# Performance work log

Hardware: AMD Instinct MI355X
Metric: run time of the kernel (lower is better)

Reference implementation:

```python
import jax, jax.numpy as jnp
import numpy as np

NUM_LAYERS = 3
BUFFER_SIZE = 5
RECENCY = 0.9
LOW_POWER_K = 8

B, N, S, C = 8, 8192, 64, 16


def setup_inputs() -> dict:
    key = jax.random.key(0)
    ks = jax.random.split(key, 8)
    return {
        "x": jax.random.normal(ks[0], (B, N, S), jnp.float32),
        "entanglement": jax.random.normal(ks[1], (N, S), jnp.float32),
        # mixing initialized as identity in the module; perturb slightly so it is non-trivial
        "mixing": jnp.eye(N, dtype=jnp.float32) + 0.01 * jax.random.normal(ks[2], (N, N), jnp.float32),
        "readout_w": jax.random.normal(ks[3], (S, S), jnp.float32) / np.sqrt(S).astype(np.float32),
        "enc_w": jax.random.normal(ks[4], (C, S), jnp.float32) / np.sqrt(S).astype(np.float32),
        "enc_b": jnp.zeros((C,), jnp.float32),
        "dec_w": jax.random.normal(ks[5], (S, C), jnp.float32) / np.sqrt(C).astype(np.float32),
        "dec_b": jnp.zeros((S,), jnp.float32),
    }


def _temporal_proximity_scaling(stack, recency_factor):
    # stack: [T, N, S] of buffered activations, stack[-1] most recent.
    # Recency-weighted mean: most recent weight 1, older decayed by recency_factor.
    T = stack.shape[0]
    w = recency_factor ** jnp.arange(T - 1, -1, -1, dtype=stack.dtype)  # [T]
    return jnp.einsum('t,tns->ns', w, stack) / jnp.sum(w)


def _low_power_collapse(s, k):
    # keep top-k |values| per neuron row, zero the rest
    a = jnp.abs(s)
    vals, _ = jax.lax.top_k(a, k)           # [N, k]
    thr = vals[:, -1:]                       # kth largest magnitude per row
    return jnp.where(a >= thr, s, jnp.zeros_like(s))


def reference(x, entanglement, mixing, readout_w, enc_w, enc_b, dec_w, dec_b):
    gate = jax.nn.sigmoid(entanglement)[None]  # [1, N, S]
    buf = []  # ShortTermBuffer contents, vectorized over all neurons: list of [N, S]
    ns = jnp.zeros((N, S), x.dtype)
    for _ in range(NUM_LAYERS):
        # NOTE: the torch code prunes/decays/resets neuron_states at the top of each
        # layer but immediately overwrites it with x.mean(0) -> dead code, omitted.
        x = x * gate
        x = jnp.einsum('bns,nm->bms', x, mixing)
        ns = jnp.mean(x, axis=0)  # [N, S]
        buf.append(ns)
        buf = buf[-BUFFER_SIZE:]
        stack = jnp.stack(buf, axis=0)        # [T, N, S], T = min(layer+1, BUFFER_SIZE)
        ns = _temporal_proximity_scaling(stack, RECENCY)
        # advanced_state_collapse via autoencoder (importance_threshold=0.0 -> always reconstruct)
        h = jax.nn.relu(ns @ enc_w.T + enc_b)  # [N, C]
        ns = h @ dec_w.T + dec_b               # [N, S]
        ns = _low_power_collapse(ns, LOW_POWER_K)
    out = x @ readout_w.T  # Linear(S, S, bias=False)
    # torch forward returns only readout(x); neuron_states is a mutated buffer.
    # We also return it so the memory-bound per-neuron state pipeline is not DCE'd.
    return out, ns
```

## Files before the change

kernel.cpp:

```cpp
#include <hip/hip_runtime.h>

#define NN 8192
#define SS 64
#define BSD 512
#define NS (NN*SS)
#define NBS (NN*BSD)

typedef __attribute__((ext_vector_type(4))) _Float16 f16x4;
typedef __attribute__((ext_vector_type(8))) _Float16 f16x8;
typedef __attribute__((ext_vector_type(4))) float f32x4;

#define GLOAD_LDS16(gptr, lptr) \
    __builtin_amdgcn_global_load_lds((const __attribute__((address_space(1))) void*)(gptr), \
                                     (__attribute__((address_space(3))) void*)(lptr), 16, 0, 0)

__device__ __forceinline__ int kmap(int lane, int e) {
    return ((lane >> 4) << 2) + (e & 3) + ((e >> 2) << 4);
}

__global__ void sigmoid_gate_kernel(const float* __restrict__ ent, float* __restrict__ gate) {
    int i = blockIdx.x * 256 + threadIdx.x;
    gate[i] = 1.0f / (1.0f + expf(-ent[i]));
}

__global__ __launch_bounds__(256) void convA_kernel(const float* __restrict__ Mx,
                                                    char* __restrict__ Ab) {
    __shared__ _Float16 Lh[64][136];
    __shared__ _Float16 Ll[64][136];
    const int t = threadIdx.x;
    const int kt = blockIdx.x, mt = blockIdx.y;
    const int k0 = kt * 64, m0 = mt * 128;
    #pragma unroll
    for (int i = 0; i < 8; ++i) {
        int e = i * 256 + t;
        int kr = e >> 5, m4 = (e & 31) << 2;
        float4 v = *(const float4*)&Mx[(size_t)(k0 + kr) * NN + m0 + m4];
        int d = (k0 + kr) - (m0 + m4);
        if (d == 0) v.x -= 1.0f;
        if (d == 1) v.y -= 1.0f;
        if (d == 2) v.z -= 1.0f;
        if (d == 3) v.w -= 1.0f;
        f16x4 h, l;
        h[0] = (_Float16)v.x; l[0] = (_Float16)(v.x - (float)h[0]);
        h[1] = (_Float16)v.y; l[1] = (_Float16)(v.y - (float)h[1]);
        h[2] = (_Float16)v.z; l[2] = (_Float16)(v.z - (float)h[2]);
        h[3] = (_Float16)v.w; l[3] = (_Float16)(v.w - (float)h[3]);
        *(f16x4*)&Lh[kr][m4] = h;
        *(f16x4*)&Ll[kr][m4] = l;
    }
    __syncthreads();
    #pragma unroll
    for (int j = 0; j < 4; ++j) {
        int idx  = j * 256 + t;
        int h    = idx >> 9;
        int w    = idx & 511;
        int blk  = w >> 7;
        int kk   = (w >> 6) & 1;
        int lane = w & 63;
        int col  = h * 64 + blk * 16 + (lane & 15);
        int kb   = kk * 32;
        f16x8 hv, lv;
        #pragma unroll
        for (int e = 0; e < 8; ++e) {
            int k = kb + kmap(lane, e);
            hv[e] = Lh[k][col];
            lv[e] = Ll[k][col];
        }
        char* tile = Ab + (((size_t)(mt * 2 + h) * 128 + kt) << 14);
        *(f16x8*)(tile + w * 16)        = hv;
        *(f16x8*)(tile + 8192 + w * 16) = lv;
    }
}

__device__ __forceinline__ void pack_B(const _Float16 (*Lh)[520],
                                       const _Float16 (*Nh)[72], const _Float16 (*Nl)[72],
                                       char* Bb, char* Nb, int kt, int t) {
    #pragma unroll
    for (int j = 0; j < 16; ++j) {
        int idx = j * 256 + t;
        int nbt = idx >> 10, w = idx & 1023;
        int blk = w >> 7, kk = (w >> 6) & 1, lane = w & 63;
        int col = nbt * 128 + blk * 16 + (lane & 15);
        int kb = kk * 32;
        f16x8 hv;
        #pragma unroll
        for (int e = 0; e < 8; ++e)
            hv[e] = Lh[kb + kmap(lane, e)][col];
        *(f16x8*)(Bb + (((size_t)kt * 4 + nbt) << 14) + w * 16) = hv;
    }
    #pragma unroll
    for (int j = 0; j < 4; ++j) {
        int idx = j * 256 + t;
        int nbt = idx >> 8, r = idx & 255;
        int part = r >> 7, kk = (r >> 6) & 1, lane = r & 63;
        int s = nbt * 16 + (lane & 15);
        int kb = kk * 32;
        f16x8 v;
        #pragma unroll
        for (int e = 0; e < 8; ++e) {
            int k = kb + kmap(lane, e);
            v[e] = part ? Nl[k][s] : Nh[k][s];
        }
        *(f16x8*)(Nb + (((size_t)kt * 4 + nbt) << 12) + part * 2048 + kk * 1024 + lane * 16) = v;
    }
}

__global__ __launch_bounds__(256) void prep0_kernel(const float* __restrict__ x,
                                                    const float* __restrict__ gate,
                                                    float* __restrict__ X,
                                                    char* __restrict__ Bb,
                                                    char* __restrict__ Nb,
                                                    float* __restrict__ mg32) {
    __shared__ _Float16 Lh[64][520];
    __shared__ _Float16 Nh[64][72];
    __shared__ _Float16 Nl[64][72];
    const int t = threadIdx.x;
    const int kt = blockIdx.x;
    const int n0 = kt * 64;
    #pragma unroll
    for (int i = 0; i < 4; ++i) {
        int e = i * 256 + t;
        int kr = e >> 4;
        int s4 = (e & 15) << 2;
        float4 g = *(const float4*)&gate[(size_t)(n0 + kr) * 64 + s4];
        float4 ms = make_float4(0.f, 0.f, 0.f, 0.f);
        #pragma unroll
        for (int b = 0; b < 8; ++b) {
            float4 v = *(const float4*)&x[((size_t)b * NN + n0 + kr) * 64 + s4];
            ms.x += v.x; ms.y += v.y; ms.z += v.z; ms.w += v.w;
            v.x *= g.x; v.y *= g.y; v.z *= g.z; v.w *= g.w;
            *(float4*)&X[(size_t)(n0 + kr) * BSD + b * 64 + s4] = v;
            f16x4 h;
            h[0] = (_Float16)v.x; h[1] = (_Float16)v.y;
            h[2] = (_Float16)v.z; h[3] = (_Float16)v.w;
            *(f16x4*)&Lh[kr][b * 64 + s4] = h;
        }
        float4 mg4;
        mg4.x = ms.x * 0.125f * g.x; mg4.y = ms.y * 0.125f * g.y;
        mg4.z = ms.z * 0.125f * g.z; mg4.w = ms.w * 0.125f * g.w;
        *(float4*)&mg32[(size_t)(n0 + kr) * 64 + s4] = mg4;
        f16x4 mh, ml;
        mh[0] = (_Float16)mg4.x; ml[0] = (_Float16)(mg4.x - (float)mh[0]);
        mh[1] = (_Float16)mg4.y; ml[1] = (_Float16)(mg4.y - (float)mh[1]);
        mh[2] = (_Float16)mg4.z; ml[2] = (_Float16)(mg4.z - (float)mh[2]);
        mh[3] = (_Float16)mg4.w; ml[3] = (_Float16)(mg4.w - (float)mh[3]);
        *(f16x4*)&Nh[kr][s4] = mh;
        *(f16x4*)&Nl[kr][s4] = ml;
    }
    __syncthreads();
    pack_B(Lh, Nh, Nl, Bb, Nb, kt, t);
}

__global__ __launch_bounds__(256) void gateconv_kernel(float* __restrict__ X,
                                                       const float* __restrict__ gate,
                                                       const float* __restrict__ nsprev,
                                                       char* __restrict__ Bb,
                                                       char* __restrict__ Nb,
                                                       float* __restrict__ mg32) {
    __shared__ _Float16 Lh[64][520];
    __shared__ _Float16 Nh[64][72];
    __shared__ _Float16 Nl[64][72];
    const int t = threadIdx.x;
    const int kt = blockIdx.x;
    const int n0 = kt * 64;
    #pragma unroll
    for (int i = 0; i < 32; ++i) {
        int e = i * 256 + t;
        int kr = e >> 7;
        int c4 = (e & 127) << 2;
        float4 v = *(const float4*)&X[(size_t)(n0 + kr) * BSD + c4];
        float4 g = *(const float4*)&gate[(size_t)(n0 + kr) * 64 + (c4 & 63)];
        v.x *= g.x; v.y *= g.y; v.z *= g.z; v.w *= g.w;
        *(float4*)&X[(size_t)(n0 + kr) * BSD + c4] = v;
        f16x4 h;
        h[0] = (_Float16)v.x; h[1] = (_Float16)v.y;
        h[2] = (_Float16)v.z; h[3] = (_Float16)v.w;
        *(f16x4*)&Lh[kr][c4] = h;
    }
    #pragma unroll
    for (int i = 0; i < 4; ++i) {
        int e = i * 256 + t;
        int kr = e >> 4;
        int s4 = (e & 15) << 2;
        float4 p = *(const float4*)&nsprev[(size_t)(n0 + kr) * 64 + s4];
        float4 g = *(const float4*)&gate[(size_t)(n0 + kr) * 64 + s4];
        float4 mg4;
        mg4.x = p.x * g.x; mg4.y = p.y * g.y; mg4.z = p.z * g.z; mg4.w = p.w * g.w;
        *(float4*)&mg32[(size_t)(n0 + kr) * 64 + s4] = mg4;
        f16x4 mh, ml;
        mh[0] = (_Float16)mg4.x; ml[0] = (_Float16)(mg4.x - (float)mh[0]);
        mh[1] = (_Float16)mg4.y; ml[1] = (_Float16)(mg4.y - (float)mh[1]);
        mh[2] = (_Float16)mg4.z; ml[2] = (_Float16)(mg4.z - (float)mh[2]);
        mh[3] = (_Float16)mg4.w; ml[3] = (_Float16)(mg4.w - (float)mh[3]);
        *(f16x4*)&Nh[kr][s4] = mh;
        *(f16x4*)&Nl[kr][s4] = ml;
    }
    __syncthreads();
    pack_B(Lh, Nh, Nl, Bb, Nb, kt, t);
}

__global__ __launch_bounds__(256) void gemm_f16_kernel(const char* __restrict__ Ab,
                                                       const char* __restrict__ Bb,
                                                       const char* __restrict__ Nb,
                                                       float* X,
                                                       const float* __restrict__ mg,
                                                       float* __restrict__ nsout) {
    __shared__ char lds[2][20480];
    const int t = threadIdx.x;
    const int L = blockIdx.x;
    const int mt  = (L & 7) + ((L >> 5) << 3);
    const int nbt = (L >> 3) & 3;
    const int lane = t & 63, wid = t >> 6;

    const char* gA = Ab + (((size_t)mt * 128) << 14) + wid * 2048 + lane * 16;
    const char* gB = Bb + (((size_t)nbt) << 14) + wid * 4096 + lane * 16;
    const char* gN = Nb + (((size_t)nbt) << 12) + wid * 1024 + lane * 16;
    const uint32_t lA = wid * 2048;
    const uint32_t lN = 16384 + wid * 1024;

    auto stageA = [&](char* la, const char* pA, const char* pN) {
        GLOAD_LDS16(pA,               la + lA);
        GLOAD_LDS16(pA + 1024,        la + lA + 1024);
        GLOAD_LDS16(pA + 8192,        la + lA + 8192);
        GLOAD_LDS16(pA + 8192 + 1024, la + lA + 8192 + 1024);
        GLOAD_LDS16(pN,               la + lN);
    };

    f16x8 B0[4], B1[4];
    auto loadB = [&](f16x8* Br, const char* pB) {
        Br[0] = *(const f16x8*)(pB);
        Br[1] = *(const f16x8*)(pB + 1024);
        Br[2] = *(const f16x8*)(pB + 2048);
        Br[3] = *(const f16x8*)(pB + 3072);
    };

    f32x4 accm[4][2];
    #pragma unroll
    for (int fi = 0; fi < 4; ++fi) {
        accm[fi][0] = (f32x4){0.f, 0.f, 0.f, 0.f};
        accm[fi][1] = (f32x4){0.f, 0.f, 0.f, 0.f};
    }
    f32x4 accn = (f32x4){0.f, 0.f, 0.f, 0.f};

    auto compute = [&](const char* base, const f16x8* Br) {
        const char* A_ = base + lane * 16;
        const char* Bn = base + 16384 + lane * 16;
        #pragma unroll
        for (int kk = 0; kk < 2; ++kk) {
            const int ko = kk * 1024;
            f16x8 bnh = *(const f16x8*)(Bn + ko);
            f16x8 bnl = *(const f16x8*)(Bn + 2048 + ko);
            #pragma unroll
            for (int fi = 0; fi < 4; ++fi) {
                f16x8 ah = *(const f16x8*)(A_ + fi * 2048 + ko);
                accm[fi][0] = __builtin_amdgcn_mfma_f32_16x16x32_f16(ah, Br[kk],     accm[fi][0], 0, 0, 0);
                accm[fi][1] = __builtin_amdgcn_mfma_f32_16x16x32_f16(ah, Br[2 + kk], accm[fi][1], 0, 0, 0);
                if (fi == wid) {
                    f16x8 aln = *(const f16x8*)(A_ + 8192 + fi * 2048 + ko);
                    accn = __builtin_amdgcn_mfma_f32_16x16x32_f16(ah,  bnh, accn, 0, 0, 0);
                    accn = __builtin_amdgcn_mfma_f32_16x16x32_f16(ah,  bnl, accn, 0, 0, 0);
                    accn = __builtin_amdgcn_mfma_f32_16x16x32_f16(aln, bnh, accn, 0, 0, 0);
                }
            }
        }
    };

    stageA(lds[0], gA, gN);
    loadB(B0, gB);
    gA += 16384; gN += 16384; gB += 65536;

    for (int u = 0; u < 64; ++u) {
        asm volatile("s_waitcnt vmcnt(0)" ::: "memory");
        __builtin_amdgcn_s_barrier();
        __builtin_amdgcn_sched_barrier(0);
        stageA(lds[1], gA, gN);
        loadB(B1, gB);
        gA += 16384; gN += 16384; gB += 65536;
        __builtin_amdgcn_sched_barrier(0);
        compute(lds[0], B0);
        asm volatile("s_waitcnt vmcnt(0)" ::: "memory");
        __builtin_amdgcn_s_barrier();
        __builtin_amdgcn_sched_barrier(0);
        if (u < 63) {
            stageA(lds[0], gA, gN);
            loadB(B0, gB);
            gA += 16384; gN += 16384; gB += 65536;
        }
        __builtin_amdgcn_sched_barrier(0);
        compute(lds[1], B1);
    }

    const int row0 = mt * 64 + ((lane >> 4) << 2);
    const int col0 = nbt * 128 + wid * 32 + (lane & 15);
    #pragma unroll
    for (int fi = 0; fi < 4; ++fi)
        #pragma unroll
        for (int fj = 0; fj < 2; ++fj)
            #pragma unroll
            for (int j = 0; j < 4; ++j) {
                size_t idx = (size_t)(row0 + fi * 16 + j) * BSD + col0 + fj * 16;
                X[idx] = accm[fi][fj][j] + X[idx];
            }
    const int nr0 = mt * 64 + wid * 16 + ((lane >> 4) << 2);
    const int nc  = nbt * 16 + (lane & 15);
    #pragma unroll
    for (int j = 0; j < 4; ++j) {
        size_t nidx = (size_t)(nr0 + j) * 64 + nc;
        nsout[nidx] = accn[j] + mg[nidx];
    }
}

__global__ __launch_bounds__(256) void readout_kernel(const float* __restrict__ X3,
                                                      const float* __restrict__ W,
                                                      float* __restrict__ out) {
    __shared__ float Wt[64][65];
    __shared__ float xr[512];
    const int n = blockIdx.x;
    const int t = threadIdx.x;
    for (int e = t; e < 4096; e += 256) {
        int s = e >> 6, sp = e & 63;
        Wt[sp][s] = W[e];
    }
    xr[t]       = X3[(size_t)n * BSD + t];
    xr[t + 256] = X3[(size_t)n * BSD + 256 + t];
    __syncthreads();
    const int b1 = t >> 6;
    const int s  = t & 63;
    float acc0 = 0.0f, acc1 = 0.0f;
    #pragma unroll
    for (int sp = 0; sp < 64; ++sp) {
        float w = Wt[sp][s];
        acc0 += w * xr[b1 * 64 + sp];
        acc1 += w * xr[(b1 + 4) * 64 + sp];
    }
    out[((size_t)b1 * NN + n) * SS + s]       = acc0;
    out[((size_t)(b1 + 4) * NN + n) * SS + s] = acc1;
}

__global__ void nsfinal_kernel(const float* __restrict__ ns0,
                               const float* __restrict__ enc_w, const float* __restrict__ enc_b,
                               const float* __restrict__ dec_w, const float* __restrict__ dec_b,
                               float* __restrict__ out_ns) {
    int gtid = blockIdx.x * 256 + threadIdx.x;
    int lane = gtid & 63;
    const float r = 0.9f;
    const float wsum = 1.0f + r + r * r;
    float tns = (ns0[gtid] * (r * r) + ns0[NS + gtid] * r + ns0[2 * NS + gtid]) / wsum;
    float v = dec_b[lane];
    #pragma unroll
    for (int c = 0; c < 16; ++c) {
        float p = tns * enc_w[c * 64 + lane];
        #pragma unroll
        for (int off = 32; off; off >>= 1) p += __shfl_xor(p, off, 64);
        float h = fmaxf(p + enc_b[c], 0.0f);
        v += h * dec_w[lane * 16 + c];
    }
    float av = fabsf(v);
    int cnt = 0;
    for (int j = 0; j < 64; ++j) {
        float o = __shfl(av, j, 64);
        cnt += (o > av) ? 1 : 0;
    }
    out_ns[gtid] = (cnt < 8) ? v : 0.0f;
}

extern "C" void kernel_launch(void* const* d_in, const int* in_sizes, int n_in,
                              void* d_out, int out_size, void* d_ws, size_t ws_size,
                              hipStream_t stream) {
    const float* x      = (const float*)d_in[0];
    const float* ent    = (const float*)d_in[1];
    const float* mixing = (const float*)d_in[2];
    const float* r_w    = (const float*)d_in[3];
    const float* enc_w  = (const float*)d_in[4];
    const float* enc_b  = (const float*)d_in[5];
    const float* dec_w  = (const float*)d_in[6];
    const float* dec_b  = (const float*)d_in[7];
    float* out = (float*)d_out;

    char*  Ab   = (char*)d_ws;
    char*  Bb   = Ab + 268435456ull;
    char*  Nb   = Bb + 8388608ull;
    float* X    = (float*)(Nb + 2097152ull);
    float* mg32 = X + NBS;
    float* ns0  = mg32 + NS;
    float* gate = ns0 + 3 * (size_t)NS;

    sigmoid_gate_kernel<<<NS / 256, 256, 0, stream>>>(ent, gate);
    convA_kernel<<<dim3(128, 64), 256, 0, stream>>>(mixing, Ab);
    prep0_kernel<<<128, 256, 0, stream>>>(x, gate, X, Bb, Nb, mg32);

    for (int l = 0; l < 3; ++l) {
        gemm_f16_kernel<<<512, 256, 0, stream>>>(Ab, Bb, Nb, X, mg32, ns0 + (size_t)l * NS);
        if (l < 2)
            gateconv_kernel<<<128, 256, 0, stream>>>(X, gate, ns0 + (size_t)l * NS, Bb, Nb, mg32);
    }

    readout_kernel<<<NN, 256, 0, stream>>>(X, r_w, out);
    nsfinal_kernel<<<2048, 256, 0, stream>>>(ns0, enc_w, enc_b, dec_w, dec_b, out + NBS);
}
```

Measured before the change: 702.9 us.

## Split-K the mixing GEMM into two partial halves reduced downstream

Each layer's mixing GEMM is split along K into two halves, launched as 1024 blocks instead of 512 to raise occupancy. Each half writes fp32 partials, which the following gateconv, readout and nsfinal kernels sum together with the residual. The ns path is restructured to keep the full and low-precision halves in registers rather than LDS. This adds extra partial-buffer traffic and needs more workspace, with the old in-place path kept as a fallback when the workspace is too small.

```diff
diff --git a/kernel.cpp b/kernel.cpp
--- a/kernel.cpp
+++ b/kernel.cpp
@@ -152,11 +152,15 @@
 }
 
 __global__ __launch_bounds__(256) void gateconv_kernel(float* __restrict__ X,
+                                                       const float* __restrict__ P0,
+                                                       const float* __restrict__ P1,
                                                        const float* __restrict__ gate,
-                                                       const float* __restrict__ nsprev,
+                                                       float* __restrict__ mg32,
+                                                       const float* __restrict__ Np0,
+                                                       const float* __restrict__ Np1,
+                                                       float* __restrict__ nsf,
                                                        char* __restrict__ Bb,
-                                                       char* __restrict__ Nb,
-                                                       float* __restrict__ mg32) {
+                                                       char* __restrict__ Nb) {
     __shared__ _Float16 Lh[64][520];
     __shared__ _Float16 Nh[64][72];
     __shared__ _Float16 Nl[64][72];
@@ -168,10 +172,19 @@
         int e = i * 256 + t;
         int kr = e >> 7;
         int c4 = (e & 127) << 2;
-        float4 v = *(const float4*)&X[(size_t)(n0 + kr) * BSD + c4];
+        size_t idx = (size_t)(n0 + kr) * BSD + c4;
+        float4 v = *(const float4*)&X[idx];
+        if (P0) {
+            float4 p = *(const float4*)&P0[idx];
+            v.x += p.x; v.y += p.y; v.z += p.z; v.w += p.w;
+        }
+        if (P1) {
+            float4 p = *(const float4*)&P1[idx];
+            v.x += p.x; v.y += p.y; v.z += p.z; v.w += p.w;
+        }
         float4 g = *(const float4*)&gate[(size_t)(n0 + kr) * 64 + (c4 & 63)];
         v.x *= g.x; v.y *= g.y; v.z *= g.z; v.w *= g.w;
-        *(float4*)&X[(size_t)(n0 + kr) * BSD + c4] = v;
+        *(float4*)&X[idx] = v;
         f16x4 h;
         h[0] = (_Float16)v.x; h[1] = (_Float16)v.y;
         h[2] = (_Float16)v.z; h[3] = (_Float16)v.w;
@@ -182,11 +195,24 @@
         int e = i * 256 + t;
         int kr = e >> 4;
         int s4 = (e & 15) << 2;
-        float4 p = *(const float4*)&nsprev[(size_t)(n0 + kr) * 64 + s4];
-        float4 g = *(const float4*)&gate[(size_t)(n0 + kr) * 64 + s4];
+        size_t nidx = (size_t)(n0 + kr) * 64 + s4;
+        float4 p;
+        if (Np0) {
+            p = *(const float4*)&mg32[nidx];
+            float4 a = *(const float4*)&Np0[nidx];
+            p.x += a.x; p.y += a.y; p.z += a.z; p.w += a.w;
+            if (Np1) {
+                float4 b2 = *(const float4*)&Np1[nidx];
+                p.x += b2.x; p.y += b2.y; p.z += b2.z; p.w += b2.w;
+            }
+            *(float4*)&nsf[nidx] = p;
+        } else {
+            p = *(const float4*)&nsf[nidx];
+        }
+        float4 g = *(const float4*)&gate[nidx];
         float4 mg4;
         mg4.x = p.x * g.x; mg4.y = p.y * g.y; mg4.z = p.z * g.z; mg4.w = p.w * g.w;
-        *(float4*)&mg32[(size_t)(n0 + kr) * 64 + s4] = mg4;
+        *(float4*)&mg32[nidx] = mg4;
         f16x4 mh, ml;
         mh[0] = (_Float16)mg4.x; ml[0] = (_Float16)(mg4.x - (float)mh[0]);
         mh[1] = (_Float16)mg4.y; ml[1] = (_Float16)(mg4.y - (float)mh[1]);
@@ -199,25 +225,139 @@
     pack_B(Lh, Nh, Nl, Bb, Nb, kt, t);
 }
 
-__global__ __launch_bounds__(256) void gemm_f16_kernel(const char* __restrict__ Ab,
-                                                       const char* __restrict__ Bb,
-                                                       const char* __restrict__ Nb,
-                                                       float* X,
-                                                       const float* __restrict__ mg,
-                                                       float* __restrict__ nsout) {
+__global__ __launch_bounds__(256, 4) void gemm_split_kernel(const char* __restrict__ Ab,
+                                                            const char* __restrict__ Bb,
+                                                            const char* __restrict__ Nb,
+                                                            float* __restrict__ Pp,
+                                                            float* __restrict__ Npp) {
+    __shared__ char lds[2][16384];
+    const int t = threadIdx.x;
+    int L = blockIdx.x;
+    const int kb = L >> 9;
+    L &= 511;
+    const int mt  = (L & 7) + ((L >> 5) << 3);
+    const int nbt = (L >> 3) & 3;
+    const int lane = t & 63, wid = t >> 6;
+    const int kt0 = kb * 64;
+
+    const char* gA = Ab + (((size_t)mt * 128 + kt0) << 14) + wid * 2048 + lane * 16;
+    const char* gB = Bb + (((size_t)kt0 * 4 + nbt) << 14) + wid * 4096 + lane * 16;
+    const char* gN = Nb + (((size_t)kt0 * 4 + nbt) << 12) + lane * 16;
+    const uint32_t lA = wid * 2048;
+
+    auto stageA = [&](char* la, const char* pA) {
+        GLOAD_LDS16(pA,               la + lA);
+        GLOAD_LDS16(pA + 1024,        la + lA + 1024);
+        GLOAD_LDS16(pA + 8192,        la + lA + 8192);
+        GLOAD_LDS16(pA + 8192 + 1024, la + lA + 8192 + 1024);
+    };
+
+    f16x8 B0[4], B1[4];
+    auto loadB = [&](f16x8* Br, const char* pB) {
+        Br[0] = *(const f16x8*)(pB);
+        Br[1] = *(const f16x8*)(pB + 1024);
+        Br[2] = *(const f16x8*)(pB + 2048);
+        Br[3] = *(const f16x8*)(pB + 3072);
+    };
+    f16x8 N0[4], N1[4];
+    auto loadN = [&](f16x8* Nr, const char* pN) {
+        Nr[0] = *(const f16x8*)(pN);
+        Nr[1] = *(const f16x8*)(pN + 1024);
+        Nr[2] = *(const f16x8*)(pN + 2048);
+        Nr[3] = *(const f16x8*)(pN + 3072);
+    };
+
+    f32x4 accm[4][2];
+    #pragma unroll
+    for (int fi = 0; fi < 4; ++fi) {
+        accm[fi][0] = (f32x4){0.f, 0.f, 0.f, 0.f};
+        accm[fi][1] = (f32x4){0.f, 0.f, 0.f, 0.f};
+    }
+    f32x4 accn = (f32x4){0.f, 0.f, 0.f, 0.f};
+
+    auto compute = [&](const char* base, const f16x8* Br, const f16x8* Nr) {
+        const char* A_ = base + lane * 16;
+        #pragma unroll
+        for (int kk = 0; kk < 2; ++kk) {
+            const int ko = kk * 1024;
+            #pragma unroll
+            for (int fi = 0; fi < 4; ++fi) {
+                f16x8 ah = *(const f16x8*)(A_ + fi * 2048 + ko);
+                accm[fi][0] = __builtin_amdgcn_mfma_f32_16x16x32_f16(ah, Br[kk],     accm[fi][0], 0, 0, 0);
+                accm[fi][1] = __builtin_amdgcn_mfma_f32_16x16x32_f16(ah, Br[2 + kk], accm[fi][1], 0, 0, 0);
+                if (fi == wid) {
+                    f16x8 aln = *(const f16x8*)(A_ + 8192 + fi * 2048 + ko);
+                    accn = __builtin_amdgcn_mfma_f32_16x16x32_f16(ah,  Nr[kk],     accn, 0, 0, 0);
+                    accn = __builtin_amdgcn_mfma_f32_16x16x32_f16(ah,  Nr[2 + kk], accn, 0, 0, 0);
+                    accn = __builtin_amdgcn_mfma_f32_16x16x32_f16(aln, Nr[kk],     accn, 0, 0, 0);
+                }
+            }
+        }
+    };
+
+    stageA(lds[0], gA);
+    loadB(B0, gB);
+    loadN(N0, gN);
+    gA += 16384; gB += 65536; gN += 16384;
+
+    for (int u = 0; u < 32; ++u) {
+        asm volatile("s_waitcnt vmcnt(0)" ::: "memory");
+        __builtin_amdgcn_s_barrier();
+        __builtin_amdgcn_sched_barrier(0);
+        stageA(lds[1], gA);
+        loadB(B1, gB);
+        loadN(N1, gN);
+        gA += 16384; gB += 65536; gN += 16384;
+        __builtin_amdgcn_sched_barrier(0);
+        compute(lds[0], B0, N0);
+        asm volatile("s_waitcnt vmcnt(0)" ::: "memory");
+        __builtin_amdgcn_s_barrier();
+        __builtin_amdgcn_sched_barrier(0);
+        if (u < 31) {
+            stageA(lds[0], gA);
+            loadB(B0, gB);
+            loadN(N0, gN);
+            gA += 16384; gB += 65536; gN += 16384;
+        }
+        __builtin_amdgcn_sched_barrier(0);
+        compute(lds[1], B1, N1);
+    }
+
+    float* P  = Pp  + (size_t)kb * NBS;
+    float* Np = Npp + (size_t)kb * NS;
+    const int row0 = mt * 64 + ((lane >> 4) << 2);
+    const int col0 = nbt * 128 + wid * 32 + (lane & 15);
+    #pragma unroll
+    for (int fi = 0; fi < 4; ++fi)
+        #pragma unroll
+        for (int fj = 0; fj < 2; ++fj)
+            #pragma unroll
+            for (int j = 0; j < 4; ++j)
+                P[(size_t)(row0 + fi * 16 + j) * BSD + col0 + fj * 16] = accm[fi][fj][j];
+    const int nr0 = mt * 64 + wid * 16 + ((lane >> 4) << 2);
+    const int nc  = nbt * 16 + (lane & 15);
+    #pragma unroll
+    for (int j = 0; j < 4; ++j)
+        Np[(size_t)(nr0 + j) * 64 + nc] = accn[j];
+}
+
+__global__ __launch_bounds__(256) void gemm_inplace_kernel(const char* __restrict__ Ab,
+                                                           const char* __restrict__ Bb,
+                                                           const char* __restrict__ Nb,
+                                                           float* X,
+                                                           const float* __restrict__ mg,
+                                                           float* __restrict__ nsout) {
     __shared__ char lds[2][20480];
     const int t = threadIdx.x;
     const int L = blockIdx.x;
     const int mt  = (L & 7) + ((L >> 5) << 3);
     const int nbt = (L >> 3) & 3;
     const int lane = t & 63, wid = t >> 6;
-
     const char* gA = Ab + (((size_t)mt * 128) << 14) + wid * 2048 + lane * 16;
     const char* gB = Bb + (((size_t)nbt) << 14) + wid * 4096 + lane * 16;
     const char* gN = Nb + (((size_t)nbt) << 12) + wid * 1024 + lane * 16;
     const uint32_t lA = wid * 2048;
     const uint32_t lN = 16384 + wid * 1024;
-
     auto stageA = [&](char* la, const char* pA, const char* pN) {
         GLOAD_LDS16(pA,               la + lA);
         GLOAD_LDS16(pA + 1024,        la + lA + 1024);
@@ -225,7 +365,6 @@
         GLOAD_LDS16(pA + 8192 + 1024, la + lA + 8192 + 1024);
         GLOAD_LDS16(pN,               la + lN);
     };
-
     f16x8 B0[4], B1[4];
     auto loadB = [&](f16x8* Br, const char* pB) {
         Br[0] = *(const f16x8*)(pB);
@@ -233,7 +372,6 @@
         Br[2] = *(const f16x8*)(pB + 2048);
         Br[3] = *(const f16x8*)(pB + 3072);
     };
-
     f32x4 accm[4][2];
     #pragma unroll
     for (int fi = 0; fi < 4; ++fi) {
@@ -241,7 +379,6 @@
         accm[fi][1] = (f32x4){0.f, 0.f, 0.f, 0.f};
     }
     f32x4 accn = (f32x4){0.f, 0.f, 0.f, 0.f};
-
     auto compute = [&](const char* base, const f16x8* Br) {
         const char* A_ = base + lane * 16;
         const char* Bn = base + 16384 + lane * 16;
@@ -264,11 +401,9 @@
             }
         }
     };
-
     stageA(lds[0], gA, gN);
     loadB(B0, gB);
     gA += 16384; gN += 16384; gB += 65536;
-
     for (int u = 0; u < 64; ++u) {
         asm volatile("s_waitcnt vmcnt(0)" ::: "memory");
         __builtin_amdgcn_s_barrier();
@@ -289,7 +424,6 @@
         __builtin_amdgcn_sched_barrier(0);
         compute(lds[1], B1);
     }
-
     const int row0 = mt * 64 + ((lane >> 4) << 2);
     const int col0 = nbt * 128 + wid * 32 + (lane & 15);
     #pragma unroll
@@ -311,6 +445,8 @@
 }
 
 __global__ __launch_bounds__(256) void readout_kernel(const float* __restrict__ X3,
+                                                      const float* __restrict__ P0,
+                                                      const float* __restrict__ P1,
                                                       const float* __restrict__ W,
                                                       float* __restrict__ out) {
     __shared__ float Wt[64][65];
@@ -321,8 +457,12 @@
         int s = e >> 6, sp = e & 63;
         Wt[sp][s] = W[e];
     }
-    xr[t]       = X3[(size_t)n * BSD + t];
-    xr[t + 256] = X3[(size_t)n * BSD + 256 + t];
+    size_t i0 = (size_t)n * BSD + t;
+    size_t i1 = i0 + 256;
+    float a = X3[i0], b = X3[i1];
+    if (P0) { a += P0[i0]; b += P0[i1]; }
+    if (P1) { a += P1[i0]; b += P1[i1]; }
+    xr[t] = a; xr[t + 256] = b;
     __syncthreads();
     const int b1 = t >> 6;
     const int s  = t & 63;
@@ -337,7 +477,11 @@
     out[((size_t)(b1 + 4) * NN + n) * SS + s] = acc1;
 }
 
-__global__ void nsfinal_kernel(const float* __restrict__ ns0,
+__global__ void nsfinal_kernel(const float* __restrict__ ns1,
+                               const float* __restrict__ ns2,
+                               const float* __restrict__ mg3,
+                               const float* __restrict__ Np0,
+                               const float* __restrict__ Np1,
                                const float* __restrict__ enc_w, const float* __restrict__ enc_b,
                                const float* __restrict__ dec_w, const float* __restrict__ dec_b,
                                float* __restrict__ out_ns) {
@@ -345,7 +489,10 @@
     int lane = gtid & 63;
     const float r = 0.9f;
     const float wsum = 1.0f + r + r * r;
-    float tns = (ns0[gtid] * (r * r) + ns0[NS + gtid] * r + ns0[2 * NS + gtid]) / wsum;
+    float n3 = mg3[gtid];
+    if (Np0) n3 += Np0[gtid];
+    if (Np1) n3 += Np1[gtid];
+    float tns = (ns1[gtid] * (r * r) + ns2[gtid] * r + n3) / wsum;
     float v = dec_b[lane];
     #pragma unroll
     for (int c = 0; c < 16; ++c) {
@@ -384,17 +531,38 @@
     float* mg32 = X + NBS;
     float* ns0  = mg32 + NS;
     float* gate = ns0 + 3 * (size_t)NS;
+    float* Pp   = gate + NS;
+    float* Npp  = Pp + 2 * (size_t)NBS;
+    const size_t NEED2 = (size_t)(Npp + 2 * (size_t)NS - (float*)d_ws) * 4;
+    const bool split = ws_size >= NEED2;
 
     sigmoid_gate_kernel<<<NS / 256, 256, 0, stream>>>(ent, gate);
     convA_kernel<<<dim3(128, 64), 256, 0, stream>>>(mixing, Ab);
     prep0_kernel<<<128, 256, 0, stream>>>(x, gate, X, Bb, Nb, mg32);
 
-    for (int l = 0; l < 3; ++l) {
-        gemm_f16_kernel<<<512, 256, 0, stream>>>(Ab, Bb, Nb, X, mg32, ns0 + (size_t)l * NS);
-        if (l < 2)
-            gateconv_kernel<<<128, 256, 0, stream>>>(X, gate, ns0 + (size_t)l * NS, Bb, Nb, mg32);
-    }
-
-    readout_kernel<<<NN, 256, 0, stream>>>(X, r_w, out);
-    nsfinal_kernel<<<2048, 256, 0, stream>>>(ns0, enc_w, enc_b, dec_w, dec_b, out + NBS);
-}
+    if (split) {
+        for (int l = 0; l < 3; ++l) {
+            gemm_split_kernel<<<1024, 256, 0, stream>>>(Ab, Bb, Nb, Pp, Npp);
+            if (l < 2)
+                gateconv_kernel<<<128, 256, 0, stream>>>(X, Pp, Pp + NBS, gate, mg32,
+                                                         Npp, Npp + NS, ns0 + (size_t)l * NS,
+                                                         Bb, Nb);
+        }
+        readout_kernel<<<NN, 256, 0, stream>>>(X, Pp, Pp + NBS, r_w, out);
+        nsfinal_kernel<<<2048, 256, 0, stream>>>(ns0, ns0 + NS, mg32, Npp, Npp + NS,
+                                                 enc_w, enc_b, dec_w, dec_b, out + NBS);
+    } else {
+        for (int l = 0; l < 3; ++l) {
+            gemm_inplace_kernel<<<512, 256, 0, stream>>>(Ab, Bb, Nb, X, mg32,
+                                                         ns0 + (size_t)l * NS);
+            if (l < 2)
+                gateconv_kernel<<<128, 256, 0, stream>>>(X, nullptr, nullptr, gate, mg32,
+                                                         nullptr, nullptr, ns0 + (size_t)l * NS,
+                                                         Bb, Nb);
+        }
+        readout_kernel<<<NN, 256, 0, stream>>>(X, nullptr, nullptr, r_w, out);
+        nsfinal_kernel<<<2048, 256, 0, stream>>>(ns0, ns0 + NS, ns0 + 2 * (size_t)NS,
+                                                 nullptr, nullptr,
+                                                 enc_w, enc_b, dec_w, dec_b, out + NBS);
+    }
+}
```

Result: slower. 806.7 us (+14.8%).

## Halve GEMM column tile, double grid, and relax pipeline waits to partial vmcnt

Applied to the files above, without the earlier changes.

Each GEMM block now covers 64 output columns instead of 128, and the grid grows from 512 to 1024 blocks. Only half the blocks compute the neuron-state side product. The prefetch is issued before the wait, which now uses a partial vmcnt so the next stage's loads stay in flight during compute, and launch_bounds requests 4 blocks per multiprocessor. The aim is more parallelism and better latency hiding, at the cost of re-reading the A tiles twice as often and adding extra barriers.

```diff
diff --git a/kernel.cpp b/kernel.cpp
--- a/kernel.cpp
+++ b/kernel.cpp
@@ -199,63 +199,57 @@
     pack_B(Lh, Nh, Nl, Bb, Nb, kt, t);
 }
 
-__global__ __launch_bounds__(256) void gemm_f16_kernel(const char* __restrict__ Ab,
-                                                       const char* __restrict__ Bb,
-                                                       const char* __restrict__ Nb,
-                                                       float* X,
-                                                       const float* __restrict__ mg,
-                                                       float* __restrict__ nsout) {
+__global__ __launch_bounds__(256, 4) void gemm_f16_kernel(const char* __restrict__ Ab,
+                                                          const char* __restrict__ Bb,
+                                                          const char* __restrict__ Nb,
+                                                          float* X,
+                                                          const float* __restrict__ mg,
+                                                          float* __restrict__ nsout) {
     __shared__ char lds[2][20480];
     const int t = threadIdx.x;
     const int L = blockIdx.x;
-    const int mt  = (L & 7) + ((L >> 5) << 3);
-    const int nbt = (L >> 3) & 3;
+    const int mt = (L & 7) | ((L >> 6) << 3);
+    const int cb = (L >> 3) & 7;
     const int lane = t & 63, wid = t >> 6;
+    const bool hasNs = (cb < 4);
 
     const char* gA = Ab + (((size_t)mt * 128) << 14) + wid * 2048 + lane * 16;
-    const char* gB = Bb + (((size_t)nbt) << 14) + wid * 4096 + lane * 16;
-    const char* gN = Nb + (((size_t)nbt) << 12) + wid * 1024 + lane * 16;
+    const char* gB = Bb + (((size_t)(cb >> 1)) << 14) + ((cb & 1) * 4 + wid) * 2048 + lane * 16;
+    const char* gN = Nb + (((size_t)(cb & 3)) << 12) + wid * 1024 + lane * 16;
     const uint32_t lA = wid * 2048;
     const uint32_t lN = 16384 + wid * 1024;
 
-    auto stageA = [&](char* la, const char* pA, const char* pN) {
-        GLOAD_LDS16(pA,               la + lA);
-        GLOAD_LDS16(pA + 1024,        la + lA + 1024);
-        GLOAD_LDS16(pA + 8192,        la + lA + 8192);
-        GLOAD_LDS16(pA + 8192 + 1024, la + lA + 8192 + 1024);
-        GLOAD_LDS16(pN,               la + lN);
+    f16x8 B0[2], B1[2];
+
+    auto stage = [&](char* la, f16x8* Br) {
+        GLOAD_LDS16(gA,               la + lA);
+        GLOAD_LDS16(gA + 1024,        la + lA + 1024);
+        GLOAD_LDS16(gA + 8192,        la + lA + 8192);
+        GLOAD_LDS16(gA + 8192 + 1024, la + lA + 8192 + 1024);
+        if (hasNs) GLOAD_LDS16(gN,    la + lN);
+        Br[0] = *(const f16x8*)(gB);
+        Br[1] = *(const f16x8*)(gB + 1024);
+        gA += 16384; gB += 65536; gN += 16384;
     };
 
-    f16x8 B0[4], B1[4];
-    auto loadB = [&](f16x8* Br, const char* pB) {
-        Br[0] = *(const f16x8*)(pB);
-        Br[1] = *(const f16x8*)(pB + 1024);
-        Br[2] = *(const f16x8*)(pB + 2048);
-        Br[3] = *(const f16x8*)(pB + 3072);
-    };
-
-    f32x4 accm[4][2];
-    #pragma unroll
-    for (int fi = 0; fi < 4; ++fi) {
-        accm[fi][0] = (f32x4){0.f, 0.f, 0.f, 0.f};
-        accm[fi][1] = (f32x4){0.f, 0.f, 0.f, 0.f};
-    }
+    f32x4 accm[4];
+    #pragma unroll
+    for (int fi = 0; fi < 4; ++fi) accm[fi] = (f32x4){0.f, 0.f, 0.f, 0.f};
     f32x4 accn = (f32x4){0.f, 0.f, 0.f, 0.f};
 
     auto compute = [&](const char* base, const f16x8* Br) {
         const char* A_ = base + lane * 16;
-        const char* Bn = base + 16384 + lane * 16;
+        const char* N_ = base + 16384 + lane * 16;
         #pragma unroll
         for (int kk = 0; kk < 2; ++kk) {
             const int ko = kk * 1024;
-            f16x8 bnh = *(const f16x8*)(Bn + ko);
-            f16x8 bnl = *(const f16x8*)(Bn + 2048 + ko);
             #pragma unroll
             for (int fi = 0; fi < 4; ++fi) {
                 f16x8 ah = *(const f16x8*)(A_ + fi * 2048 + ko);
-                accm[fi][0] = __builtin_amdgcn_mfma_f32_16x16x32_f16(ah, Br[kk],     accm[fi][0], 0, 0, 0);
-                accm[fi][1] = __builtin_amdgcn_mfma_f32_16x16x32_f16(ah, Br[2 + kk], accm[fi][1], 0, 0, 0);
-                if (fi == wid) {
+                accm[fi] = __builtin_amdgcn_mfma_f32_16x16x32_f16(ah, Br[kk], accm[fi], 0, 0, 0);
+                if (hasNs && fi == wid) {
+                    f16x8 bnh = *(const f16x8*)(N_ + ko);
+                    f16x8 bnl = *(const f16x8*)(N_ + 2048 + ko);
                     f16x8 aln = *(const f16x8*)(A_ + 8192 + fi * 2048 + ko);
                     accn = __builtin_amdgcn_mfma_f32_16x16x32_f16(ah,  bnh, accn, 0, 0, 0);
                     accn = __builtin_amdgcn_mfma_f32_16x16x32_f16(ah,  bnl, accn, 0, 0, 0);
@@ -265,48 +259,45 @@
         }
     };
 
-    stageA(lds[0], gA, gN);
-    loadB(B0, gB);
-    gA += 16384; gN += 16384; gB += 65536;
-
+#define WAIT_PREV() do { if (hasNs) asm volatile("s_waitcnt vmcnt(7)" ::: "memory"); \
+                         else       asm volatile("s_waitcnt vmcnt(6)" ::: "memory"); } while (0)
+
+    stage(lds[0], B0);
     for (int u = 0; u < 64; ++u) {
-        asm volatile("s_waitcnt vmcnt(0)" ::: "memory");
+        stage(lds[1], B1);
+        WAIT_PREV();
         __builtin_amdgcn_s_barrier();
-        __builtin_amdgcn_sched_barrier(0);
-        stageA(lds[1], gA, gN);
-        loadB(B1, gB);
-        gA += 16384; gN += 16384; gB += 65536;
-        __builtin_amdgcn_sched_barrier(0);
         compute(lds[0], B0);
-        asm volatile("s_waitcnt vmcnt(0)" ::: "memory");
         __builtin_amdgcn_s_barrier();
-        __builtin_amdgcn_sched_barrier(0);
         if (u < 63) {
-            stageA(lds[0], gA, gN);
-            loadB(B0, gB);
-            gA += 16384; gN += 16384; gB += 65536;
-        }
-        __builtin_amdgcn_sched_barrier(0);
+            stage(lds[0], B0);
+            WAIT_PREV();
+        } else {
+            asm volatile("s_waitcnt vmcnt(0)" ::: "memory");
+        }
+        __builtin_amdgcn_s_barrier();
         compute(lds[1], B1);
-    }
+        __builtin_amdgcn_s_barrier();
+    }
+#undef WAIT_PREV
 
     const int row0 = mt * 64 + ((lane >> 4) << 2);
-    const int col0 = nbt * 128 + wid * 32 + (lane & 15);
+    const int col0 = cb * 64 + wid * 16 + (lane & 15);
     #pragma unroll
     for (int fi = 0; fi < 4; ++fi)
         #pragma unroll
-        for (int fj = 0; fj < 2; ++fj)
-            #pragma unroll
-            for (int j = 0; j < 4; ++j) {
-                size_t idx = (size_t)(row0 + fi * 16 + j) * BSD + col0 + fj * 16;
-                X[idx] = accm[fi][fj][j] + X[idx];
-            }
-    const int nr0 = mt * 64 + wid * 16 + ((lane >> 4) << 2);
-    const int nc  = nbt * 16 + (lane & 15);
-    #pragma unroll
-    for (int j = 0; j < 4; ++j) {
-        size_t nidx = (size_t)(nr0 + j) * 64 + nc;
-        nsout[nidx] = accn[j] + mg[nidx];
+        for (int j = 0; j < 4; ++j) {
+            size_t idx = (size_t)(row0 + fi * 16 + j) * BSD + col0;
+            X[idx] = accm[fi][j] + X[idx];
+        }
+    if (hasNs) {
+        const int nr0 = mt * 64 + wid * 16 + ((lane >> 4) << 2);
+        const int nc  = cb * 16 + (lane & 15);
+        #pragma unroll
+        for (int j = 0; j < 4; ++j) {
+            size_t nidx = (size_t)(nr0 + j) * 64 + nc;
+            nsout[nidx] = accn[j] + mg[nidx];
+        }
     }
 }
 
@@ -390,7 +381,7 @@
     prep0_kernel<<<128, 256, 0, stream>>>(x, gate, X, Bb, Nb, mg32);
 
     for (int l = 0; l < 3; ++l) {
-        gemm_f16_kernel<<<512, 256, 0, stream>>>(Ab, Bb, Nb, X, mg32, ns0 + (size_t)l * NS);
+        gemm_f16_kernel<<<1024, 256, 0, stream>>>(Ab, Bb, Nb, X, mg32, ns0 + (size_t)l * NS);
         if (l < 2)
             gateconv_kernel<<<128, 256, 0, stream>>>(X, gate, ns0 + (size_t)l * NS, Bb, Nb, mg32);
     }
```

Result: slower. 782.9 us (+11.4%).
